# Optimization experiments

Hardware: AMD Instinct MI355X
Metric: run time of the kernel (lower is better)

## Reference

```python
import jax, jax.numpy as jnp
import numpy as np

B, S, D, H, L = 2, 4096, 768, 12, 12
DH = D // H
BS = 16                # block size
NB = S // BS           # 256 blocks
NR = 2                 # random blocks per middle query block
DFF = 3072
VOCAB = 50358


def layer_norm(x, s, b):
    m = x.mean(-1, keepdims=True)
    v = ((x - m) ** 2).mean(-1, keepdims=True)
    return (x - m) * jax.lax.rsqrt(v + 1e-12) * s + b


def setup_inputs() -> dict:
    key = jax.random.key(0)
    ks = jax.random.split(key, 20)
    rn = lambda k, shp: jax.random.normal(k, shp, jnp.float32) * 0.02
    # random key-block indices per middle query block, avoiding window+global blocks
    rng = np.random.default_rng(0)
    rb = np.zeros((NB - 2, NR), np.int32)
    for i in range(1, NB - 1):
        forbidden = {0, i - 1, i, i + 1, NB - 1}
        choices = np.array([b for b in range(NB) if b not in forbidden])
        rb[i - 1] = rng.choice(choices, NR, replace=False)
    return {
        "input_ids": jax.random.randint(ks[0], (B, S), 0, VOCAB, jnp.int32),
        "rand_blocks": jnp.asarray(rb),
        "emb_word": rn(ks[1], (VOCAB, D)),
        "emb_pos": rn(ks[2], (S, D)),
        "ln0_s": jnp.ones((D,)), "ln0_b": jnp.zeros((D,)),
        "Wq": rn(ks[3], (L, D, D)), "bq": jnp.zeros((L, D)),
        "Wk": rn(ks[4], (L, D, D)), "bk": jnp.zeros((L, D)),
        "Wv": rn(ks[5], (L, D, D)), "bv": jnp.zeros((L, D)),
        "Wo": rn(ks[6], (L, D, D)), "bo": jnp.zeros((L, D)),
        "ln1_s": jnp.ones((L, D)), "ln1_b": jnp.zeros((L, D)),
        "W1": rn(ks[7], (L, D, DFF)), "b1": jnp.zeros((L, DFF)),
        "W2": rn(ks[8], (L, DFF, D)), "b2": jnp.zeros((L, D)),
        "ln2_s": jnp.ones((L, D)), "ln2_b": jnp.zeros((L, D)),
        "Wp": rn(ks[9], (D, D)), "bp": jnp.zeros((D,)),
        "start_w": jax.random.normal(ks[10], (D,), jnp.float32),
        "end_w": jax.random.normal(ks[11], (D,), jnp.float32),
        "Wd1": rn(ks[12], (D, 20)), "bd1": jnp.zeros((20,)),
        "Wd2": rn(ks[13], (20, 2)), "bd2": jnp.zeros((2,)),
    }


def block_sparse_attn(h, wq, bq_, wk, bk_, wv, bv_, wo, bo_, rand_blocks):
    scale = 1.0 / np.sqrt(DH)
    heads = lambda w, b: (h @ w + b).reshape(B, S, H, DH).transpose(0, 2, 1, 3)
    q = heads(wq, bq_) * scale
    k = heads(wk, bk_)
    v = heads(wv, bv_)
    qb = q.reshape(B, H, NB, BS, DH)
    kb = k.reshape(B, H, NB, BS, DH)
    vb = v.reshape(B, H, NB, BS, DH)
    # global query blocks (first & last) attend to every key
    qg = qb[:, :, jnp.array([0, NB - 1])]                       # [B,H,2,BS,DH]
    ag = jax.nn.softmax(jnp.einsum('bhgqd,bhkd->bhgqk', qg, k), -1)
    og = jnp.einsum('bhgqk,bhkd->bhgqd', ag, v)
    # middle query blocks: global(2) + window(3) + random(2) key blocks
    mid = jnp.arange(1, NB - 1, dtype=jnp.int32)
    idx = jnp.concatenate([
        jnp.zeros((NB - 2, 1), jnp.int32),
        jnp.full((NB - 2, 1), NB - 1, jnp.int32),
        jnp.stack([mid - 1, mid, mid + 1], -1),
        rand_blocks.astype(jnp.int32),
    ], axis=1)                                                  # [NB-2, 7]
    kg = kb[:, :, idx].reshape(B, H, NB - 2, 7 * BS, DH)        # gathered keys
    vg = vb[:, :, idx].reshape(B, H, NB - 2, 7 * BS, DH)
    qm = qb[:, :, 1:NB - 1]                                     # [B,H,NB-2,BS,DH]
    am = jax.nn.softmax(jnp.einsum('bhnqd,bhnkd->bhnqk', qm, kg), -1)
    om = jnp.einsum('bhnqk,bhnkd->bhnqd', am, vg)
    ob = jnp.concatenate([og[:, :, :1], om, og[:, :, 1:]], axis=2)  # [B,H,NB,BS,DH]
    o = ob.reshape(B, H, S, DH).transpose(0, 2, 1, 3).reshape(B, S, D)
    return o @ wo + bo_


def encoder(input_ids, rand_blocks, emb_word, emb_pos, ln0_s, ln0_b,
            Wq, bq, Wk, bk, Wv, bv, Wo, bo, ln1_s, ln1_b,
            W1, b1, W2, b2, ln2_s, ln2_b):
    h = layer_norm(emb_word[input_ids] + emb_pos[None], ln0_s, ln0_b)

    def layer(hc, p):
        wq, bq_, wk, bk_, wv, bv_, wo, bo_, l1s, l1b, w1, b1_, w2, b2_, l2s, l2b = p
        a = block_sparse_attn(hc, wq, bq_, wk, bk_, wv, bv_, wo, bo_, rand_blocks)
        hc = layer_norm(hc + a, l1s, l1b)
        f = jax.nn.gelu(hc @ w1 + b1_, approximate=False) @ w2 + b2_
        hc = layer_norm(hc + f, l2s, l2b)
        return hc, None

    h, _ = jax.lax.scan(layer, h, (Wq, bq, Wk, bk, Wv, bv, Wo, bo,
                                   ln1_s, ln1_b, W1, b1, W2, b2, ln2_s, ln2_b))
    return h


def reference(input_ids, rand_blocks, emb_word, emb_pos, ln0_s, ln0_b,
              Wq, bq, Wk, bk, Wv, bv, Wo, bo, ln1_s, ln1_b,
              W1, b1, W2, b2, ln2_s, ln2_b, Wp, bp,
              start_w, end_w, Wd1, bd1, Wd2, bd2):
    h = encoder(input_ids, rand_blocks, emb_word, emb_pos, ln0_s, ln0_b,
                Wq, bq, Wk, bk, Wv, bv, Wo, bo, ln1_s, ln1_b,
                W1, b1, W2, b2, ln2_s, ln2_b)
    start_logits = h @ start_w        # [B,S]
    end_logits = h @ end_w            # [B,S]
    pooled = jnp.tanh(h[:, 0] @ Wp + bp)   # BERT-style pooler on [CLS]
    d1 = jax.nn.relu(pooled @ Wd1 + bd1)
    disc_logits = d1 @ Wd2 + bd2      # [B,2]
    return start_logits, end_logits, disc_logits
```

## Files before the change

### kernel.cpp

```cpp
#include <hip/hip_runtime.h>

#define DEV __device__ __forceinline__

typedef unsigned short u16;
typedef short bf16x8 __attribute__((ext_vector_type(8)));
typedef float f32x4 __attribute__((ext_vector_type(4)));

constexpr int Bc = 2, Sc = 4096, Dc = 768, Hc = 12, Lc = 12;
constexpr int BSc = 16, NBc = 256, NRc = 2, DFFc = 3072;
constexpr int Mr = Bc * Sc;

DEV u16 f2b(float f) {
  unsigned u = __builtin_bit_cast(unsigned, f);
  u += 0x7fffu + ((u >> 16) & 1u);
  return (u16)(u >> 16);
}
DEV float b2f(u16 u) { return __builtin_bit_cast(float, (unsigned)u << 16); }

DEV void gload_lds16(const void* g, void* l) {
  __builtin_amdgcn_global_load_lds((const __attribute__((address_space(1))) void*)g,
                                   (__attribute__((address_space(3))) void*)l, 16, 0, 0);
}

template<int EPI>
__global__ __launch_bounds__(512, 1)
void gemmP(const u16* __restrict__ A, const u16* __restrict__ Bt,
           const float* __restrict__ bias, u16* __restrict__ Cb,
           float* __restrict__ Cf,
           u16* __restrict__ Qh, u16* __restrict__ Kh, u16* __restrict__ Vh,
           u16* __restrict__ VhT, int M, int N, int K)
{
  __shared__ u16 As[2][128 * 64];
  __shared__ u16 Bs[2][256 * 64];
  const int tid = threadIdx.x;
  const int wid = tid >> 6, lane = tid & 63;
  const int fr = lane & 15, fq = lane >> 4;
  const int wr = wid >> 2, wc = wid & 3;

  int nwg = gridDim.x * gridDim.y;
  int orig = blockIdx.y * gridDim.x + blockIdx.x;
  int swz = (nwg & 7) ? orig : (orig & 7) * (nwg >> 3) + (orig >> 3);
  int bx = swz % gridDim.x, by = swz / gridDim.x;
  const int m0 = by * 128, n0 = bx * 256;

  const u16* asrc[2];
  const u16* bsrc[4];
#pragma unroll
  for (int p = 0; p < 2; ++p) {
    int ci = p * 512 + tid;
    int r = ci >> 3, c = (ci & 7) ^ (r & 7);
    asrc[p] = A + (size_t)(m0 + r) * K + c * 8;
  }
#pragma unroll
  for (int p = 0; p < 4; ++p) {
    int ci = p * 512 + tid;
    int r = ci >> 3, c = (ci & 7) ^ (r & 7);
    bsrc[p] = Bt + (size_t)(n0 + r) * K + c * 8;
  }
  auto stageA = [&](int buf, int k0) {
#pragma unroll
    for (int p = 0; p < 2; ++p)
      gload_lds16(asrc[p] + k0, &As[buf][(p * 512 + tid) * 8]);
  };
  auto stageB = [&](int buf, int k0) {
#pragma unroll
    for (int p = 0; p < 4; ++p)
      gload_lds16(bsrc[p] + k0, &Bs[buf][(p * 512 + tid) * 8]);
  };

  f32x4 acc[4][4] = {};
  const int arow = wr * 64 + fr;
  const int brow = wc * 64 + fr;

  stageA(0, 0);  stageB(0, 0);
  stageA(1, 64); stageB(1, 64);
  asm volatile("s_waitcnt vmcnt(6)" ::: "memory");
  __builtin_amdgcn_sched_barrier(0);
  __builtin_amdgcn_s_barrier();

  const int nt = K >> 6;
  for (int kt = 0; kt < nt; ++kt) {
    const u16* ab = As[kt & 1];
    const u16* bb = Bs[kt & 1];
    bf16x8 aA[2][2], aB[2][2], bA[2][2], bB[2][2];

#pragma unroll
    for (int f = 0; f < 2; ++f)
#pragma unroll
      for (int kh = 0; kh < 2; ++kh) {
        int rowa = arow + f * 16;
        aA[f][kh] = *(const bf16x8*)(ab + rowa * 64 + (((kh * 4 + fq) ^ (rowa & 7)) << 3));
        int rowb = brow + f * 16;
        bA[f][kh] = *(const bf16x8*)(bb + rowb * 64 + (((kh * 4 + fq) ^ (rowb & 7)) << 3));
      }
    __builtin_amdgcn_s_setprio(1);
#pragma unroll
    for (int m = 0; m < 2; ++m)
#pragma unroll
      for (int n = 0; n < 2; ++n)
#pragma unroll
        for (int kh = 0; kh < 2; ++kh)
          acc[m][n] = __builtin_amdgcn_mfma_f32_16x16x32_bf16(aA[m][kh], bA[n][kh], acc[m][n], 0, 0, 0);
    __builtin_amdgcn_s_setprio(0);

#pragma unroll
    for (int f = 0; f < 2; ++f)
#pragma unroll
      for (int kh = 0; kh < 2; ++kh) {
        int rowb = brow + 32 + f * 16;
        bB[f][kh] = *(const bf16x8*)(bb + rowb * 64 + (((kh * 4 + fq) ^ (rowb & 7)) << 3));
      }
    __builtin_amdgcn_s_setprio(1);
#pragma unroll
    for (int m = 0; m < 2; ++m)
#pragma unroll
      for (int n = 0; n < 2; ++n)
#pragma unroll
        for (int kh = 0; kh < 2; ++kh)
          acc[m][n + 2] = __builtin_amdgcn_mfma_f32_16x16x32_bf16(aA[m][kh], bB[n][kh], acc[m][n + 2], 0, 0, 0);
    __builtin_amdgcn_s_setprio(0);
    asm volatile("s_waitcnt lgkmcnt(0)" ::: "memory");
    __builtin_amdgcn_sched_barrier(0);
    __builtin_amdgcn_s_barrier();

    if (kt + 2 < nt) stageB(kt & 1, (kt + 2) * 64);
#pragma unroll
    for (int f = 0; f < 2; ++f)
#pragma unroll
      for (int kh = 0; kh < 2; ++kh) {
        int rowa = arow + 32 + f * 16;
        aB[f][kh] = *(const bf16x8*)(ab + rowa * 64 + (((kh * 4 + fq) ^ (rowa & 7)) << 3));
      }
    __builtin_amdgcn_s_setprio(1);
#pragma unroll
    for (int m = 0; m < 2; ++m)
#pragma unroll
      for (int n = 0; n < 2; ++n)
#pragma unroll
        for (int kh = 0; kh < 2; ++kh)
          acc[m + 2][n] = __builtin_amdgcn_mfma_f32_16x16x32_bf16(aB[m][kh], bA[n][kh], acc[m + 2][n], 0, 0, 0);
    __builtin_amdgcn_s_setprio(0);
    asm volatile("s_waitcnt lgkmcnt(0)" ::: "memory");
    __builtin_amdgcn_sched_barrier(0);
    __builtin_amdgcn_s_barrier();

    if (kt + 2 < nt) stageA(kt & 1, (kt + 2) * 64);
    __builtin_amdgcn_s_setprio(1);
#pragma unroll
    for (int m = 0; m < 2; ++m)
#pragma unroll
      for (int n = 0; n < 2; ++n)
#pragma unroll
        for (int kh = 0; kh < 2; ++kh)
          acc[m + 2][n + 2] = __builtin_amdgcn_mfma_f32_16x16x32_bf16(aB[m][kh], bB[n][kh], acc[m + 2][n + 2], 0, 0, 0);
    __builtin_amdgcn_s_setprio(0);
    if (kt + 1 < nt) {
      if (kt + 2 < nt) asm volatile("s_waitcnt vmcnt(6)" ::: "memory");
      else             asm volatile("s_waitcnt vmcnt(0)" ::: "memory");
      __builtin_amdgcn_sched_barrier(0);
      __builtin_amdgcn_s_barrier();
    }
  }

#pragma unroll
  for (int m = 0; m < 4; ++m) {
#pragma unroll
    for (int n = 0; n < 4; ++n) {
      int col = n0 + wc * 64 + n * 16 + fr;
      float bv = bias[col];
      if constexpr (EPI == 2) {
        int sec = col / 768;
        int c = col - sec * 768;
        int hh = c >> 6, dd = c & 63;
#pragma unroll
        for (int r = 0; r < 4; ++r) {
          int row = m0 + wr * 64 + m * 16 + fq * 4 + r;
          int bb2 = row >> 12, ss = row & 4095;
          size_t bhh = (size_t)(bb2 * Hc + hh);
          u16 val = f2b(acc[m][n][r] + bv);
          if (sec == 0) Qh[(bhh * Sc + ss) * 64 + dd] = val;
          else if (sec == 1) Kh[(bhh * Sc + ss) * 64 + dd] = val;
          else { Vh[(bhh * Sc + ss) * 64 + dd] = val; VhT[(bhh * 64 + dd) * Sc + ss] = val; }
        }
      } else if constexpr (EPI == 1) {
#pragma unroll
        for (int r = 0; r < 4; ++r) {
          int row = m0 + wr * 64 + m * 16 + fq * 4 + r;
          float v = acc[m][n][r] + bv;
          v = 0.5f * v * (1.f + erff(v * 0.70710678118654752f));
          Cb[(size_t)row * N + col] = f2b(v);
        }
      } else {
#pragma unroll
        for (int r = 0; r < 4; ++r) {
          int row = m0 + wr * 64 + m * 16 + fq * 4 + r;
          Cf[(size_t)row * N + col] = acc[m][n][r] + bv;
        }
      }
    }
  }
}

__global__ __launch_bounds__(256, 2)
void gemmQ(const u16* __restrict__ A, const u16* __restrict__ Bt,
           const float* __restrict__ bias, float* __restrict__ Cf,
           int M, int N, int K)
{
  __shared__ u16 As[2][128 * 64];
  __shared__ u16 Bs[2][128 * 64];
  const int tid = threadIdx.x;
  const int wid = tid >> 6, lane = tid & 63;
  const int fr = lane & 15, fq = lane >> 4;
  const int wr = wid >> 1, wc = wid & 1;

  int nwg = gridDim.x * gridDim.y;
  int orig = blockIdx.y * gridDim.x + blockIdx.x;
  int swz = (nwg & 7) ? orig : (orig & 7) * (nwg >> 3) + (orig >> 3);
  int bx = swz % gridDim.x, by = swz / gridDim.x;
  const int m0 = by * 128, n0 = bx * 128;

  const u16* asrc[4];
  const u16* bsrc[4];
#pragma unroll
  for (int p = 0; p < 4; ++p) {
    int ci = p * 256 + tid;
    int r = ci >> 3, c = (ci & 7) ^ (r & 7);
    asrc[p] = A + (size_t)(m0 + r) * K + c * 8;
    bsrc[p] = Bt + (size_t)(n0 + r) * K + c * 8;
  }
  auto stageA = [&](int buf, int k0) {
#pragma unroll
    for (int p = 0; p < 4; ++p)
      gload_lds16(asrc[p] + k0, &As[buf][(p * 256 + tid) * 8]);
  };
  auto stageB = [&](int buf, int k0) {
#pragma unroll
    for (int p = 0; p < 4; ++p)
      gload_lds16(bsrc[p] + k0, &Bs[buf][(p * 256 + tid) * 8]);
  };

  f32x4 acc[4][4] = {};
  const int arow = wr * 64 + fr;
  const int brow = wc * 64 + fr;

  stageA(0, 0);  stageB(0, 0);
  stageA(1, 64); stageB(1, 64);
  asm volatile("s_waitcnt vmcnt(8)" ::: "memory");
  __builtin_amdgcn_sched_barrier(0);
  __builtin_amdgcn_s_barrier();

  const int nt = K >> 6;
  for (int kt = 0; kt < nt; ++kt) {
    const u16* ab = As[kt & 1];
    const u16* bb = Bs[kt & 1];
    bf16x8 aA[2][2], aB[2][2], bA[2][2], bB[2][2];

#pragma unroll
    for (int f = 0; f < 2; ++f)
#pragma unroll
      for (int kh = 0; kh < 2; ++kh) {
        int rowa = arow + f * 16;
        aA[f][kh] = *(const bf16x8*)(ab + rowa * 64 + (((kh * 4 + fq) ^ (rowa & 7)) << 3));
        int rowb = brow + f * 16;
        bA[f][kh] = *(const bf16x8*)(bb + rowb * 64 + (((kh * 4 + fq) ^ (rowb & 7)) << 3));
      }
    __builtin_amdgcn_s_setprio(1);
#pragma unroll
    for (int m = 0; m < 2; ++m)
#pragma unroll
      for (int n = 0; n < 2; ++n)
#pragma unroll
        for (int kh = 0; kh < 2; ++kh)
          acc[m][n] = __builtin_amdgcn_mfma_f32_16x16x32_bf16(aA[m][kh], bA[n][kh], acc[m][n], 0, 0, 0);
    __builtin_amdgcn_s_setprio(0);

#pragma unroll
    for (int f = 0; f < 2; ++f)
#pragma unroll
      for (int kh = 0; kh < 2; ++kh) {
        int rowb = brow + 32 + f * 16;
        bB[f][kh] = *(const bf16x8*)(bb + rowb * 64 + (((kh * 4 + fq) ^ (rowb & 7)) << 3));
      }
    __builtin_amdgcn_s_setprio(1);
#pragma unroll
    for (int m = 0; m < 2; ++m)
#pragma unroll
      for (int n = 0; n < 2; ++n)
#pragma unroll
        for (int kh = 0; kh < 2; ++kh)
          acc[m][n + 2] = __builtin_amdgcn_mfma_f32_16x16x32_bf16(aA[m][kh], bB[n][kh], acc[m][n + 2], 0, 0, 0);
    __builtin_amdgcn_s_setprio(0);
    asm volatile("s_waitcnt lgkmcnt(0)" ::: "memory");
    __builtin_amdgcn_sched_barrier(0);
    __builtin_amdgcn_s_barrier();

    if (kt + 2 < nt) stageB(kt & 1, (kt + 2) * 64);
#pragma unroll
    for (int f = 0; f < 2; ++f)
#pragma unroll
      for (int kh = 0; kh < 2; ++kh) {
        int rowa = arow + 32 + f * 16;
        aB[f][kh] = *(const bf16x8*)(ab + rowa * 64 + (((kh * 4 + fq) ^ (rowa & 7)) << 3));
      }
    __builtin_amdgcn_s_setprio(1);
#pragma unroll
    for (int m = 0; m < 2; ++m)
#pragma unroll
      for (int n = 0; n < 2; ++n)
#pragma unroll
        for (int kh = 0; kh < 2; ++kh)
          acc[m + 2][n] = __builtin_amdgcn_mfma_f32_16x16x32_bf16(aB[m][kh], bA[n][kh], acc[m + 2][n], 0, 0, 0);
    __builtin_amdgcn_s_setprio(0);
    asm volatile("s_waitcnt lgkmcnt(0)" ::: "memory");
    __builtin_amdgcn_sched_barrier(0);
    __builtin_amdgcn_s_barrier();

    if (kt + 2 < nt) stageA(kt & 1, (kt + 2) * 64);
    __builtin_amdgcn_s_setprio(1);
#pragma unroll
    for (int m = 0; m < 2; ++m)
#pragma unroll
      for (int n = 0; n < 2; ++n)
#pragma unroll
        for (int kh = 0; kh < 2; ++kh)
          acc[m + 2][n + 2] = __builtin_amdgcn_mfma_f32_16x16x32_bf16(aB[m][kh], bB[n][kh], acc[m + 2][n + 2], 0, 0, 0);
    __builtin_amdgcn_s_setprio(0);
    if (kt + 1 < nt) {
      if (kt + 2 < nt) asm volatile("s_waitcnt vmcnt(8)" ::: "memory");
      else             asm volatile("s_waitcnt vmcnt(0)" ::: "memory");
      __builtin_amdgcn_sched_barrier(0);
      __builtin_amdgcn_s_barrier();
    }
  }

#pragma unroll
  for (int m = 0; m < 4; ++m) {
#pragma unroll
    for (int n = 0; n < 4; ++n) {
      int col = n0 + wc * 64 + n * 16 + fr;
      float bv = bias[col];
#pragma unroll
      for (int r = 0; r < 4; ++r) {
        int row = m0 + wr * 64 + m * 16 + fq * 4 + r;
        Cf[(size_t)row * N + col] = acc[m][n][r] + bv;
      }
    }
  }
}

__global__ void wtrans_all(const float* __restrict__ Wq, const float* __restrict__ Wk,
                           const float* __restrict__ Wv, const float* __restrict__ Wo,
                           const float* __restrict__ W1, const float* __restrict__ W2,
                           u16* __restrict__ wqkvT, u16* __restrict__ woT,
                           u16* __restrict__ w1T, u16* __restrict__ w2T)
{
  int bx = blockIdx.x;
  size_t l = blockIdx.y;
  size_t wsq = l * 768 * 768, wff = l * 768 * 3072;
  const float* in; u16* out; int K, N, ntx, t; float scale = 1.f;
  if (bx < 576)       { in = Wq + wsq; out = wqkvT + l * 2304 * 768;           K = 768;  N = 768;  ntx = 24; t = bx;        scale = 0.125f; }
  else if (bx < 1152) { in = Wk + wsq; out = wqkvT + l * 2304 * 768 + 589824;  K = 768;  N = 768;  ntx = 24; t = bx - 576;  }
  else if (bx < 1728) { in = Wv + wsq; out = wqkvT + l * 2304 * 768 + 1179648; K = 768;  N = 768;  ntx = 24; t = bx - 1152; }
  else if (bx < 2304) { in = Wo + wsq; out = woT + l * 768 * 768;              K = 768;  N = 768;  ntx = 24; t = bx - 1728; }
  else if (bx < 4608) { in = W1 + wff; out = w1T + l * 3072 * 768;             K = 768;  N = 3072; ntx = 96; t = bx - 2304; }
  else                { in = W2 + wff; out = w2T + l * 768 * 3072;             K = 3072; N = 768;  ntx = 24; t = bx - 4608; }
  int n0 = (t % ntx) * 32, k0 = (t / ntx) * 32;
  __shared__ float tl[32][33];
  int tx = threadIdx.x, ty = threadIdx.y;
#pragma unroll
  for (int yy = 0; yy < 32; yy += 8)
    tl[ty + yy][tx] = in[(size_t)(k0 + ty + yy) * N + n0 + tx];
  __syncthreads();
#pragma unroll
  for (int yy = 0; yy < 32; yy += 8)
    out[(size_t)(n0 + ty + yy) * K + k0 + tx] = f2b(tl[tx][ty + yy] * scale);
}

__global__ void pack_bias(const float* __restrict__ bq, const float* __restrict__ bk,
                          const float* __restrict__ bv, float* __restrict__ bqkv)
{
  int i = blockIdx.x * 256 + threadIdx.x;
  if (i >= Lc * 2304) return;
  int l = i / 2304, j = i % 2304;
  float v = (j < 768) ? bq[(size_t)l * 768 + j] * 0.125f
          : (j < 1536) ? bk[(size_t)l * 768 + j - 768]
                       : bv[(size_t)l * 768 + j - 1536];
  bqkv[i] = v;
}

DEV void breduce2(float& a, float& b) {
  __shared__ float ra[4], rbv[4];
  for (int off = 32; off > 0; off >>= 1) {
    a += __shfl_down(a, off);
    b += __shfl_down(b, off);
  }
  int lane = threadIdx.x & 63, wid = threadIdx.x >> 6;
  if (lane == 0) { ra[wid] = a; rbv[wid] = b; }
  __syncthreads();
  a = ra[0] + ra[1] + ra[2] + ra[3];
  b = rbv[0] + rbv[1] + rbv[2] + rbv[3];
}

__global__ __launch_bounds__(256)
void embed_ln(const int* __restrict__ ids, const float* __restrict__ ew,
              const float* __restrict__ ep, const float* __restrict__ gs,
              const float* __restrict__ gb, float* __restrict__ hout, u16* __restrict__ hb)
{
  int row = blockIdx.x;
  int spos = row & (Sc - 1);
  int id = ids[row];
  int tid = threadIdx.x;
  float x[3], sum = 0.f, ss = 0.f;
#pragma unroll
  for (int j = 0; j < 3; ++j) {
    int i = tid + j * 256;
    x[j] = ew[(size_t)id * Dc + i] + ep[(size_t)spos * Dc + i];
    sum += x[j]; ss += x[j] * x[j];
  }
  breduce2(sum, ss);
  float mean = sum * (1.f / Dc);
  float var = ss * (1.f / Dc) - mean * mean;
  float inv = rsqrtf(var + 1e-12f);
#pragma unroll
  for (int j = 0; j < 3; ++j) {
    int i = tid + j * 256;
    float y = (x[j] - mean) * inv * gs[i] + gb[i];
    hout[(size_t)row * Dc + i] = y;
    hb[(size_t)row * Dc + i] = f2b(y);
  }
}

__global__ __launch_bounds__(256)
void ln_res(const float* X, const float* R, const float* gs, const float* gb,
            float* Yf, u16* Yb)
{
  int row = blockIdx.x;
  int tid = threadIdx.x;
  float x[3], sum = 0.f, ss = 0.f;
#pragma unroll
  for (int j = 0; j < 3; ++j) {
    int i = tid + j * 256;
    x[j] = X[(size_t)row * Dc + i] + R[(size_t)row * Dc + i];
    sum += x[j]; ss += x[j] * x[j];
  }
  breduce2(sum, ss);
  float mean = sum * (1.f / Dc);
  float var = ss * (1.f / Dc) - mean * mean;
  float inv = rsqrtf(var + 1e-12f);
#pragma unroll
  for (int j = 0; j < 3; ++j) {
    int i = tid + j * 256;
    float y = (x[j] - mean) * inv * gs[i] + gb[i];
    Yf[(size_t)row * Dc + i] = y;
    Yb[(size_t)row * Dc + i] = f2b(y);
  }
}

__global__ __launch_bounds__(256)
void gattn_flash(const u16* __restrict__ Qh, const u16* __restrict__ Kh,
                 const u16* __restrict__ VhT, float* __restrict__ part)
{
  __shared__ u16 pb[4][16 * 136];
  __shared__ float ob[4][16][64];
  __shared__ float mlb[4][2][16];
  const int kc = blockIdx.x, g = blockIdx.y, bh = blockIdx.z;
  const int wid = threadIdx.x >> 6, lane = threadIdx.x & 63;
  const int fr = lane & 15, fq = lane >> 4;
  const int qrow = g ? (NBc - 1) * BSc : 0;

  const u16* Qb = Qh + ((size_t)bh * Sc + qrow) * 64;
  const u16* Kb = Kh + (size_t)bh * Sc * 64;
  const u16* Vt = VhT + (size_t)bh * 64 * Sc;

  bf16x8 qa0 = *(const bf16x8*)(Qb + fr * 64 + fq * 8);
  bf16x8 qa1 = *(const bf16x8*)(Qb + fr * 64 + 32 + fq * 8);

  float m[4], l[4];
  f32x4 o[4] = {};
#pragma unroll
  for (int r = 0; r < 4; ++r) { m[r] = -3.4e38f; l[r] = 0.f; }

  u16* pbw = pb[wid];
  const int s0w = kc * 256 + wid * 64;

  for (int it = 0; it < 2; ++it) {
    const int sb = s0w + it * 32;
    f32x4 s[2];
#pragma unroll
    for (int t = 0; t < 2; ++t) {
      const u16* kr = Kb + (size_t)(sb + t * 16 + fr) * 64 + fq * 8;
      bf16x8 kb0 = *(const bf16x8*)(kr);
      bf16x8 kb1 = *(const bf16x8*)(kr + 32);
      f32x4 a = {};
      a = __builtin_amdgcn_mfma_f32_16x16x32_bf16(qa0, kb0, a, 0, 0, 0);
      a = __builtin_amdgcn_mfma_f32_16x16x32_bf16(qa1, kb1, a, 0, 0, 0);
      s[t] = a;
    }
#pragma unroll
    for (int r = 0; r < 4; ++r) {
      float pm = fmaxf(s[0][r], s[1][r]);
#pragma unroll
      for (int off = 1; off < 16; off <<= 1) pm = fmaxf(pm, __shfl_xor(pm, off));
      float nm = fmaxf(m[r], pm);
      float sc = __expf(m[r] - nm);
      m[r] = nm;
      float e0 = __expf(s[0][r] - nm), e1 = __expf(s[1][r] - nm);
      float ps = e0 + e1;
#pragma unroll
      for (int off = 1; off < 16; off <<= 1) ps += __shfl_xor(ps, off);
      l[r] = l[r] * sc + ps;
#pragma unroll
      for (int nn = 0; nn < 4; ++nn) o[nn][r] *= sc;
      pbw[(fq * 4 + r) * 136 + fr] = f2b(e0);
      pbw[(fq * 4 + r) * 136 + 16 + fr] = f2b(e1);
    }
    asm volatile("s_waitcnt lgkmcnt(0)" ::: "memory");
    __builtin_amdgcn_sched_barrier(0);
    bf16x8 pa = *(const bf16x8*)(pbw + fr * 136 + fq * 8);
#pragma unroll
    for (int nn = 0; nn < 4; ++nn) {
      bf16x8 vb = *(const bf16x8*)(Vt + (size_t)(nn * 16 + fr) * Sc + sb + fq * 8);
      o[nn] = __builtin_amdgcn_mfma_f32_16x16x32_bf16(pa, vb, o[nn], 0, 0, 0);
    }
  }

#pragma unroll
  for (int nn = 0; nn < 4; ++nn)
#pragma unroll
    for (int r = 0; r < 4; ++r)
      ob[wid][fq * 4 + r][nn * 16 + fr] = o[nn][r];
  if (fr == 0) {
#pragma unroll
    for (int r = 0; r < 4; ++r) {
      mlb[wid][0][fq * 4 + r] = m[r];
      mlb[wid][1][fq * 4 + r] = l[r];
    }
  }
  __syncthreads();

  float* pp = part + (size_t)(((bh * 2 + g) * 16) + kc) * 1056;
  int tid = threadIdx.x;
#pragma unroll
  for (int k = 0; k < 4; ++k) {
    int oidx = tid + k * 256;
    int q = oidx >> 6, d = oidx & 63;
    float M = fmaxf(fmaxf(mlb[0][0][q], mlb[1][0][q]), fmaxf(mlb[2][0][q], mlb[3][0][q]));
    float O = 0.f, L = 0.f;
#pragma unroll
    for (int w = 0; w < 4; ++w) {
      float f = __expf(mlb[w][0][q] - M);
      O += f * ob[w][q][d];
      L += f * mlb[w][1][q];
    }
    pp[q * 64 + d] = O;
    if (d == 0) { pp[1024 + q] = M; pp[1040 + q] = L; }
  }
}

__global__ __launch_bounds__(256)
void attn_tail(const u16* __restrict__ Qh, const u16* __restrict__ Kh,
               const u16* __restrict__ VhT, const int* __restrict__ rb,
               const float* __restrict__ part, u16* __restrict__ attnb)
{
  if (blockIdx.x < 48) {
    int idx = blockIdx.x;
    int bh = idx >> 1, g = idx & 1;
    int b = bh / Hc, h = bh % Hc;
    int tid = threadIdx.x;
    const float* pbase = part + (size_t)idx * 16 * 1056;
#pragma unroll
    for (int k = 0; k < 4; ++k) {
      int oidx = tid + k * 256;
      int q = oidx >> 6, d = oidx & 63;
      float M = -3.4e38f;
#pragma unroll
      for (int c = 0; c < 16; ++c) M = fmaxf(M, pbase[c * 1056 + 1024 + q]);
      float O = 0.f, L = 0.f;
#pragma unroll
      for (int c = 0; c < 16; ++c) {
        float f = __expf(pbase[c * 1056 + 1024 + q] - M);
        O += f * pbase[c * 1056 + q * 64 + d];
        L += f * pbase[c * 1056 + 1040 + q];
      }
      int srow = (g ? (NBc - 1) * BSc : 0) + q;
      attnb[((size_t)(b * Sc + srow)) * Dc + h * 64 + d] = f2b(O / L);
    }
    return;
  }

  __shared__ u16 pb[4][16 * 136];
  const int wid = threadIdx.x >> 6, lane = threadIdx.x & 63;
  const int w = (blockIdx.x - 48) * 4 + wid;
  const int n = w % 254, bh = w / 254;
  const int b = bh / Hc, h = bh % Hc;
  const int fr = lane & 15, fq = lane >> 4;

  int idx[7];
  idx[0] = 0; idx[1] = NBc - 1; idx[2] = n; idx[3] = n + 1; idx[4] = n + 2;
  idx[5] = rb[n * NRc]; idx[6] = rb[n * NRc + 1];

  const u16* Qb = Qh + ((size_t)bh * Sc + (n + 1) * BSc) * 64;
  const u16* Kb = Kh + (size_t)bh * Sc * 64;
  const u16* Vt = VhT + (size_t)bh * 64 * Sc;

  bf16x8 qa0 = *(const bf16x8*)(Qb + fr * 64 + fq * 8);
  bf16x8 qa1 = *(const bf16x8*)(Qb + fr * 64 + 32 + fq * 8);

  f32x4 s[7];
#pragma unroll
  for (int t = 0; t < 7; ++t) {
    const u16* kr = Kb + ((size_t)idx[t] * BSc + fr) * 64 + fq * 8;
    bf16x8 kb0 = *(const bf16x8*)(kr);
    bf16x8 kb1 = *(const bf16x8*)(kr + 32);
    f32x4 a = {};
    a = __builtin_amdgcn_mfma_f32_16x16x32_bf16(qa0, kb0, a, 0, 0, 0);
    a = __builtin_amdgcn_mfma_f32_16x16x32_bf16(qa1, kb1, a, 0, 0, 0);
    s[t] = a;
  }

  float mx[4], sm[4];
#pragma unroll
  for (int r = 0; r < 4; ++r) {
    mx[r] = s[0][r];
#pragma unroll
    for (int t = 1; t < 7; ++t) mx[r] = fmaxf(mx[r], s[t][r]);
  }
#pragma unroll
  for (int off = 1; off < 16; off <<= 1)
#pragma unroll
    for (int r = 0; r < 4; ++r) mx[r] = fmaxf(mx[r], __shfl_xor(mx[r], off));
#pragma unroll
  for (int r = 0; r < 4; ++r) sm[r] = 0.f;
#pragma unroll
  for (int t = 0; t < 7; ++t)
#pragma unroll
    for (int r = 0; r < 4; ++r) { float e = expf(s[t][r] - mx[r]); s[t][r] = e; sm[r] += e; }
#pragma unroll
  for (int off = 1; off < 16; off <<= 1)
#pragma unroll
    for (int r = 0; r < 4; ++r) sm[r] += __shfl_xor(sm[r], off);
  float inv[4];
#pragma unroll
  for (int r = 0; r < 4; ++r) inv[r] = 1.f / sm[r];

  u16* pbw = pb[wid];
#pragma unroll
  for (int t = 0; t < 7; ++t)
#pragma unroll
    for (int r = 0; r < 4; ++r)
      pbw[(fq * 4 + r) * 136 + t * 16 + fr] = f2b(s[t][r] * inv[r]);
  for (int i = lane; i < 16 * 24; i += 64) {
    int rr = i / 24, cc = 112 + i % 24;
    pbw[rr * 136 + cc] = 0;
  }
  __syncthreads();

  f32x4 o[4] = {};
#pragma unroll
  for (int ks = 0; ks < 4; ++ks) {
    bf16x8 pa = *(const bf16x8*)(pbw + fr * 136 + ks * 32 + fq * 8);
    int t = ks * 2 + (fq >> 1);
    int tt = (t < 7) ? t : 0;
    size_t voff = (size_t)idx[tt] * BSc + (fq & 1) * 8;
#pragma unroll
    for (int nn = 0; nn < 4; ++nn) {
      bf16x8 vb = *(const bf16x8*)(Vt + (size_t)(nn * 16 + fr) * Sc + voff);
      o[nn] = __builtin_amdgcn_mfma_f32_16x16x32_bf16(pa, vb, o[nn], 0, 0, 0);
    }
  }

  size_t rbase = (size_t)b * Sc + (n + 1) * BSc;
#pragma unroll
  for (int nn = 0; nn < 4; ++nn)
#pragma unroll
    for (int r = 0; r < 4; ++r)
      attnb[(rbase + fq * 4 + r) * Dc + h * 64 + nn * 16 + fr] = f2b(o[nn][r]);
}

__global__ __launch_bounds__(256)
void logits_k(const float* __restrict__ h, const float* __restrict__ sw,
              const float* __restrict__ ew, float* __restrict__ out)
{
  int row = blockIdx.x;
  int tid = threadIdx.x;
  float s1 = 0.f, s2 = 0.f;
#pragma unroll
  for (int j = 0; j < 3; ++j) {
    int i = tid + j * 256;
    float x = h[(size_t)row * Dc + i];
    s1 += x * sw[i]; s2 += x * ew[i];
  }
  breduce2(s1, s2);
  if (tid == 0) { out[row] = s1; out[Mr + row] = s2; }
}

__global__ __launch_bounds__(256)
void pooled_k(const float* __restrict__ h, const float* __restrict__ Wp,
              const float* __restrict__ bp, float* __restrict__ pooled)
{
  int b = blockIdx.y, j0 = blockIdx.x * 64;
  int jl = threadIdx.x & 63, kp = threadIdx.x >> 6;
  __shared__ float hr[768];
  __shared__ float part[4][64];
  for (int i = threadIdx.x; i < 768; i += 256) hr[i] = h[(size_t)b * Sc * Dc + i];
  __syncthreads();
  float a0 = 0.f, a1 = 0.f, a2 = 0.f, a3 = 0.f;
  const float* wp = Wp + (size_t)(kp * 192) * 768 + j0 + jl;
  const float* hk = hr + kp * 192;
#pragma unroll 4
  for (int k = 0; k < 192; k += 4) {
    a0 += hk[k]     * wp[(size_t)k * 768];
    a1 += hk[k + 1] * wp[(size_t)(k + 1) * 768];
    a2 += hk[k + 2] * wp[(size_t)(k + 2) * 768];
    a3 += hk[k + 3] * wp[(size_t)(k + 3) * 768];
  }
  part[kp][jl] = a0 + a1 + a2 + a3;
  __syncthreads();
  if (threadIdx.x < 64) {
    float s = part[0][jl] + part[1][jl] + part[2][jl] + part[3][jl] + bp[j0 + jl];
    pooled[b * 768 + j0 + jl] = tanhf(s);
  }
}

__global__ __launch_bounds__(256)
void head2(const float* __restrict__ pooled, const float* __restrict__ Wd1,
           const float* __restrict__ bd1, const float* __restrict__ Wd2,
           const float* __restrict__ bd2, float* __restrict__ out)
{
  __shared__ float pl[1536];
  __shared__ float part[40][6];
  __shared__ float d1[40];
  int tid = threadIdx.x;
  for (int i = tid; i < 1536; i += 256) pl[i] = pooled[i];
  __syncthreads();
  if (tid < 240) {
    int p = tid / 6, s = tid % 6;
    int b = p / 20, u = p % 20;
    float a = 0.f;
    for (int k = s * 128; k < s * 128 + 128; ++k) a += pl[b * 768 + k] * Wd1[(size_t)k * 20 + u];
    part[p][s] = a;
  }
  __syncthreads();
  if (tid < 40) {
    float a = bd1[tid % 20];
#pragma unroll
    for (int s = 0; s < 6; ++s) a += part[tid][s];
    d1[tid] = fmaxf(a, 0.f);
  }
  __syncthreads();
  if (tid < 4) {
    int b = tid >> 1, o = tid & 1;
    float a = bd2[o];
#pragma unroll
    for (int k = 0; k < 20; ++k) a += d1[b * 20 + k] * Wd2[k * 2 + o];
    out[2 * Mr + b * 2 + o] = a;
  }
}

extern "C" void kernel_launch(void* const* d_in, const int* in_sizes, int n_in,
                              void* d_out, int out_size, void* d_ws, size_t ws_size,
                              hipStream_t stream)
{
  (void)in_sizes; (void)n_in; (void)out_size; (void)ws_size;
  const int*   ids   = (const int*)d_in[0];
  const int*   rbp   = (const int*)d_in[1];
  const float* emb_w = (const float*)d_in[2];
  const float* emb_p = (const float*)d_in[3];
  const float* ln0s  = (const float*)d_in[4];
  const float* ln0b  = (const float*)d_in[5];
  const float* Wq    = (const float*)d_in[6];
  const float* bq    = (const float*)d_in[7];
  const float* Wk    = (const float*)d_in[8];
  const float* bk    = (const float*)d_in[9];
  const float* Wv    = (const float*)d_in[10];
  const float* bv    = (const float*)d_in[11];
  const float* Wo    = (const float*)d_in[12];
  const float* bo    = (const float*)d_in[13];
  const float* ln1s  = (const float*)d_in[14];
  const float* ln1b  = (const float*)d_in[15];
  const float* W1    = (const float*)d_in[16];
  const float* b1    = (const float*)d_in[17];
  const float* W2    = (const float*)d_in[18];
  const float* b2    = (const float*)d_in[19];
  const float* ln2s  = (const float*)d_in[20];
  const float* ln2b  = (const float*)d_in[21];
  const float* Wp    = (const float*)d_in[22];
  const float* bp    = (const float*)d_in[23];
  const float* sw    = (const float*)d_in[24];
  const float* ewv   = (const float*)d_in[25];
  const float* Wd1   = (const float*)d_in[26];
  const float* bd1   = (const float*)d_in[27];
  const float* Wd2   = (const float*)d_in[28];
  const float* bd2   = (const float*)d_in[29];
  float* out = (float*)d_out;

  unsigned char* pc = (unsigned char*)d_ws;
  auto carve = [&](size_t bytes) {
    void* r = (void*)pc;
    pc += (bytes + 255) & ~(size_t)255;
    return r;
  };
  u16*   wqkvT = (u16*)carve((size_t)Lc * 2304 * 768 * 2);
  u16*   woT   = (u16*)carve((size_t)Lc * 768 * 768 * 2);
  u16*   w1T   = (u16*)carve((size_t)Lc * 3072 * 768 * 2);
  u16*   w2T   = (u16*)carve((size_t)Lc * 768 * 3072 * 2);
  float* bqkv  = (float*)carve((size_t)Lc * 2304 * 4);
  float* h     = (float*)carve((size_t)Mr * Dc * 4);
  u16*   hb    = (u16*)carve((size_t)Mr * Dc * 2);
  u16*   Qh    = (u16*)carve((size_t)Mr * Dc * 2);
  u16*   Kh    = (u16*)carve((size_t)Mr * Dc * 2);
  u16*   Vh    = (u16*)carve((size_t)Mr * Dc * 2);
  u16*   VhT   = (u16*)carve((size_t)Mr * Dc * 2);
  u16*   attnb = (u16*)carve((size_t)Mr * Dc * 2);
  float* c0    = (float*)carve((size_t)Mr * Dc * 4);
  float* pool2 = (float*)carve((size_t)Bc * Dc * 4);
  float* m1ws  = (float*)carve((size_t)Mr * DFFc * 2);
  u16*   m1    = (u16*)m1ws;
  float* part  = (float*)((unsigned char*)m1ws + (size_t)13 * 1024 * 1024);

  pack_bias<<<(Lc * 2304 + 255) / 256, 256, 0, stream>>>(bq, bk, bv, bqkv);
  wtrans_all<<<dim3(6912, Lc), dim3(32, 8), 0, stream>>>(Wq, Wk, Wv, Wo, W1, W2,
                                                         wqkvT, woT, w1T, w2T);
  embed_ln<<<Mr, 256, 0, stream>>>(ids, emb_w, emb_p, ln0s, ln0b, h, hb);

  for (int l = 0; l < Lc; ++l) {
    gemmP<2><<<dim3(9, 64), 512, 0, stream>>>(hb, wqkvT + (size_t)l * 2304 * 768,
                                              bqkv + (size_t)l * 2304,
                                              nullptr, nullptr, Qh, Kh, Vh, VhT, Mr, 2304, 768);
    gattn_flash<<<dim3(16, 2, Bc * Hc), 256, 0, stream>>>(Qh, Kh, VhT, part);
    attn_tail<<<48 + 1524, 256, 0, stream>>>(Qh, Kh, VhT, rbp, part, attnb);
    gemmQ<<<dim3(6, 64), 256, 0, stream>>>(attnb, woT + (size_t)l * 768 * 768,
                                           bo + (size_t)l * 768, c0, Mr, 768, 768);
    ln_res<<<Mr, 256, 0, stream>>>(h, c0, ln1s + (size_t)l * 768, ln1b + (size_t)l * 768, h, hb);
    gemmP<1><<<dim3(12, 64), 512, 0, stream>>>(hb, w1T + (size_t)l * 3072 * 768,
                                               b1 + (size_t)l * 3072,
                                               m1, nullptr, nullptr, nullptr, nullptr, nullptr,
                                               Mr, 3072, 768);
    gemmQ<<<dim3(6, 64), 256, 0, stream>>>(m1, w2T + (size_t)l * 768 * 3072,
                                           b2 + (size_t)l * 768, c0, Mr, 768, 3072);
    ln_res<<<Mr, 256, 0, stream>>>(h, c0, ln2s + (size_t)l * 768, ln2b + (size_t)l * 768, h, hb);
  }

  logits_k<<<Mr, 256, 0, stream>>>(h, sw, ewv, out);
  pooled_k<<<dim3(12, Bc), 256, 0, stream>>>(h, Wp, bp, pool2);
  head2<<<1, 256, 0, stream>>>(pool2, Wd1, bd1, Wd2, bd2, out);
}
```

Measured before the change: 3.703 ms.

## Cut memory traffic: drop Vh, bf16 GEMM outputs, vectorize LN and weight transpose

The QKV epilogue no longer writes the unused row-major V copy, and the output-projection and FFN2 GEMMs now store bf16 instead of fp32 into the residual buffer. ln_res is rewritten to process one row per wavefront with float4/ushort4 vector loads and a shuffle-only reduction. The weight transpose kernel moves to 64x64 tiles with vectorized loads and packed stores. Rounding the residual branch to bf16 before the add loses some precision in exchange for less memory traffic.

```diff
diff --git a/kernel.cpp b/kernel.cpp
--- a/kernel.cpp
+++ b/kernel.cpp
@@ -26,8 +26,7 @@
 __global__ __launch_bounds__(512, 1)
 void gemmP(const u16* __restrict__ A, const u16* __restrict__ Bt,
            const float* __restrict__ bias, u16* __restrict__ Cb,
-           float* __restrict__ Cf,
-           u16* __restrict__ Qh, u16* __restrict__ Kh, u16* __restrict__ Vh,
+           u16* __restrict__ Qh, u16* __restrict__ Kh,
            u16* __restrict__ VhT, int M, int N, int K)
 {
   __shared__ u16 As[2][128 * 64];
@@ -180,9 +179,9 @@
           u16 val = f2b(acc[m][n][r] + bv);
           if (sec == 0) Qh[(bhh * Sc + ss) * 64 + dd] = val;
           else if (sec == 1) Kh[(bhh * Sc + ss) * 64 + dd] = val;
-          else { Vh[(bhh * Sc + ss) * 64 + dd] = val; VhT[(bhh * 64 + dd) * Sc + ss] = val; }
+          else VhT[(bhh * 64 + dd) * Sc + ss] = val;
         }
-      } else if constexpr (EPI == 1) {
+      } else {
 #pragma unroll
         for (int r = 0; r < 4; ++r) {
           int row = m0 + wr * 64 + m * 16 + fq * 4 + r;
@@ -190,12 +189,6 @@
           v = 0.5f * v * (1.f + erff(v * 0.70710678118654752f));
           Cb[(size_t)row * N + col] = f2b(v);
         }
-      } else {
-#pragma unroll
-        for (int r = 0; r < 4; ++r) {
-          int row = m0 + wr * 64 + m * 16 + fq * 4 + r;
-          Cf[(size_t)row * N + col] = acc[m][n][r] + bv;
-        }
       }
     }
   }
@@ -203,7 +196,7 @@
 
 __global__ __launch_bounds__(256, 2)
 void gemmQ(const u16* __restrict__ A, const u16* __restrict__ Bt,
-           const float* __restrict__ bias, float* __restrict__ Cf,
+           const float* __restrict__ bias, u16* __restrict__ Cb,
            int M, int N, int K)
 {
   __shared__ u16 As[2][128 * 64];
@@ -342,38 +335,47 @@
 #pragma unroll
       for (int r = 0; r < 4; ++r) {
         int row = m0 + wr * 64 + m * 16 + fq * 4 + r;
-        Cf[(size_t)row * N + col] = acc[m][n][r] + bv;
+        Cb[(size_t)row * N + col] = f2b(acc[m][n][r] + bv);
       }
     }
   }
 }
 
-__global__ void wtrans_all(const float* __restrict__ Wq, const float* __restrict__ Wk,
-                           const float* __restrict__ Wv, const float* __restrict__ Wo,
-                           const float* __restrict__ W1, const float* __restrict__ W2,
-                           u16* __restrict__ wqkvT, u16* __restrict__ woT,
-                           u16* __restrict__ w1T, u16* __restrict__ w2T)
+__global__ __launch_bounds__(256)
+void wtrans_all(const float* __restrict__ Wq, const float* __restrict__ Wk,
+                const float* __restrict__ Wv, const float* __restrict__ Wo,
+                const float* __restrict__ W1, const float* __restrict__ W2,
+                u16* __restrict__ wqkvT, u16* __restrict__ woT,
+                u16* __restrict__ w1T, u16* __restrict__ w2T)
 {
   int bx = blockIdx.x;
   size_t l = blockIdx.y;
   size_t wsq = l * 768 * 768, wff = l * 768 * 3072;
   const float* in; u16* out; int K, N, ntx, t; float scale = 1.f;
-  if (bx < 576)       { in = Wq + wsq; out = wqkvT + l * 2304 * 768;           K = 768;  N = 768;  ntx = 24; t = bx;        scale = 0.125f; }
-  else if (bx < 1152) { in = Wk + wsq; out = wqkvT + l * 2304 * 768 + 589824;  K = 768;  N = 768;  ntx = 24; t = bx - 576;  }
-  else if (bx < 1728) { in = Wv + wsq; out = wqkvT + l * 2304 * 768 + 1179648; K = 768;  N = 768;  ntx = 24; t = bx - 1152; }
-  else if (bx < 2304) { in = Wo + wsq; out = woT + l * 768 * 768;              K = 768;  N = 768;  ntx = 24; t = bx - 1728; }
-  else if (bx < 4608) { in = W1 + wff; out = w1T + l * 3072 * 768;             K = 768;  N = 3072; ntx = 96; t = bx - 2304; }
-  else                { in = W2 + wff; out = w2T + l * 768 * 3072;             K = 3072; N = 768;  ntx = 24; t = bx - 4608; }
-  int n0 = (t % ntx) * 32, k0 = (t / ntx) * 32;
-  __shared__ float tl[32][33];
-  int tx = threadIdx.x, ty = threadIdx.y;
-#pragma unroll
-  for (int yy = 0; yy < 32; yy += 8)
-    tl[ty + yy][tx] = in[(size_t)(k0 + ty + yy) * N + n0 + tx];
+  if (bx < 144)       { in = Wq + wsq; out = wqkvT + l * 2304 * 768;           K = 768;  N = 768;  ntx = 12; t = bx;        scale = 0.125f; }
+  else if (bx < 288)  { in = Wk + wsq; out = wqkvT + l * 2304 * 768 + 589824;  K = 768;  N = 768;  ntx = 12; t = bx - 144;  }
+  else if (bx < 432)  { in = Wv + wsq; out = wqkvT + l * 2304 * 768 + 1179648; K = 768;  N = 768;  ntx = 12; t = bx - 288;  }
+  else if (bx < 576)  { in = Wo + wsq; out = woT + l * 768 * 768;              K = 768;  N = 768;  ntx = 12; t = bx - 432;  }
+  else if (bx < 1152) { in = W1 + wff; out = w1T + l * 3072 * 768;             K = 768;  N = 3072; ntx = 48; t = bx - 576;  }
+  else                { in = W2 + wff; out = w2T + l * 768 * 3072;             K = 3072; N = 768;  ntx = 12; t = bx - 1152; }
+  int n0 = (t % ntx) * 64, k0 = (t / ntx) * 64;
+  __shared__ float tl[64][65];
+  int tid = threadIdx.x;
+  int kr = tid >> 4, nc = (tid & 15) * 4;
+#pragma unroll
+  for (int kk = 0; kk < 4; ++kk) {
+    float4 v = *(const float4*)(in + (size_t)(k0 + kk * 16 + kr) * N + n0 + nc);
+    float* d = &tl[kk * 16 + kr][nc];
+    d[0] = v.x; d[1] = v.y; d[2] = v.z; d[3] = v.w;
+  }
   __syncthreads();
-#pragma unroll
-  for (int yy = 0; yy < 32; yy += 8)
-    out[(size_t)(n0 + ty + yy) * K + k0 + tx] = f2b(tl[tx][ty + yy] * scale);
+  int k2 = (tid & 31) * 2, nr = tid >> 5;
+#pragma unroll
+  for (int nn = 0; nn < 8; ++nn) {
+    int n = nn * 8 + nr;
+    unsigned pk = (unsigned)f2b(tl[k2][n] * scale) | ((unsigned)f2b(tl[k2 + 1][n] * scale) << 16);
+    *(unsigned*)(out + (size_t)(n0 + n) * K + k0 + k2) = pk;
+  }
 }
 
 __global__ void pack_bias(const float* __restrict__ bq, const float* __restrict__ bk,
@@ -431,28 +433,50 @@
 }
 
 __global__ __launch_bounds__(256)
-void ln_res(const float* X, const float* R, const float* gs, const float* gb,
-            float* Yf, u16* Yb)
-{
-  int row = blockIdx.x;
-  int tid = threadIdx.x;
-  float x[3], sum = 0.f, ss = 0.f;
-#pragma unroll
-  for (int j = 0; j < 3; ++j) {
-    int i = tid + j * 256;
-    x[j] = X[(size_t)row * Dc + i] + R[(size_t)row * Dc + i];
-    sum += x[j]; ss += x[j] * x[j];
-  }
-  breduce2(sum, ss);
+void ln_res(const float* __restrict__ X, const u16* __restrict__ Rb,
+            const float* __restrict__ gs, const float* __restrict__ gb,
+            float* __restrict__ Yf, u16* __restrict__ Yb)
+{
+  const int wid = threadIdx.x >> 6, lane = threadIdx.x & 63;
+  const int row = blockIdx.x * 4 + wid;
+  const float* xr = X + (size_t)row * Dc;
+  const u16*   rr = Rb + (size_t)row * Dc;
+  float x[12];
+  float sum = 0.f, ss = 0.f;
+#pragma unroll
+  for (int p = 0; p < 3; ++p) {
+    int c = p * 256 + lane * 4;
+    float4 xv = *(const float4*)(xr + c);
+    ushort4 rv = *(const ushort4*)(rr + c);
+    float v0 = xv.x + b2f(rv.x);
+    float v1 = xv.y + b2f(rv.y);
+    float v2 = xv.z + b2f(rv.z);
+    float v3 = xv.w + b2f(rv.w);
+    x[p * 4 + 0] = v0; x[p * 4 + 1] = v1; x[p * 4 + 2] = v2; x[p * 4 + 3] = v3;
+    sum += (v0 + v1) + (v2 + v3);
+    ss  += (v0 * v0 + v1 * v1) + (v2 * v2 + v3 * v3);
+  }
+#pragma unroll
+  for (int off = 1; off < 64; off <<= 1) {
+    sum += __shfl_xor(sum, off);
+    ss  += __shfl_xor(ss, off);
+  }
   float mean = sum * (1.f / Dc);
   float var = ss * (1.f / Dc) - mean * mean;
   float inv = rsqrtf(var + 1e-12f);
 #pragma unroll
-  for (int j = 0; j < 3; ++j) {
-    int i = tid + j * 256;
-    float y = (x[j] - mean) * inv * gs[i] + gb[i];
-    Yf[(size_t)row * Dc + i] = y;
-    Yb[(size_t)row * Dc + i] = f2b(y);
+  for (int p = 0; p < 3; ++p) {
+    int c = p * 256 + lane * 4;
+    float4 gv = *(const float4*)(gs + c);
+    float4 bv = *(const float4*)(gb + c);
+    float y0 = (x[p * 4 + 0] - mean) * inv * gv.x + bv.x;
+    float y1 = (x[p * 4 + 1] - mean) * inv * gv.y + bv.y;
+    float y2 = (x[p * 4 + 2] - mean) * inv * gv.z + bv.z;
+    float y3 = (x[p * 4 + 3] - mean) * inv * gv.w + bv.w;
+    float4 yo; yo.x = y0; yo.y = y1; yo.z = y2; yo.w = y3;
+    *(float4*)(Yf + (size_t)row * Dc + c) = yo;
+    ushort4 pk; pk.x = f2b(y0); pk.y = f2b(y1); pk.z = f2b(y2); pk.w = f2b(y3);
+    *(ushort4*)(Yb + (size_t)row * Dc + c) = pk;
   }
 }
 
@@ -809,36 +833,35 @@
   u16*   hb    = (u16*)carve((size_t)Mr * Dc * 2);
   u16*   Qh    = (u16*)carve((size_t)Mr * Dc * 2);
   u16*   Kh    = (u16*)carve((size_t)Mr * Dc * 2);
-  u16*   Vh    = (u16*)carve((size_t)Mr * Dc * 2);
   u16*   VhT   = (u16*)carve((size_t)Mr * Dc * 2);
   u16*   attnb = (u16*)carve((size_t)Mr * Dc * 2);
-  float* c0    = (float*)carve((size_t)Mr * Dc * 4);
+  u16*   c0b   = (u16*)carve((size_t)Mr * Dc * 2);
   float* pool2 = (float*)carve((size_t)Bc * Dc * 4);
   float* m1ws  = (float*)carve((size_t)Mr * DFFc * 2);
   u16*   m1    = (u16*)m1ws;
   float* part  = (float*)((unsigned char*)m1ws + (size_t)13 * 1024 * 1024);
 
   pack_bias<<<(Lc * 2304 + 255) / 256, 256, 0, stream>>>(bq, bk, bv, bqkv);
-  wtrans_all<<<dim3(6912, Lc), dim3(32, 8), 0, stream>>>(Wq, Wk, Wv, Wo, W1, W2,
-                                                         wqkvT, woT, w1T, w2T);
+  wtrans_all<<<dim3(1728, Lc), 256, 0, stream>>>(Wq, Wk, Wv, Wo, W1, W2,
+                                                 wqkvT, woT, w1T, w2T);
   embed_ln<<<Mr, 256, 0, stream>>>(ids, emb_w, emb_p, ln0s, ln0b, h, hb);
 
   for (int l = 0; l < Lc; ++l) {
     gemmP<2><<<dim3(9, 64), 512, 0, stream>>>(hb, wqkvT + (size_t)l * 2304 * 768,
                                               bqkv + (size_t)l * 2304,
-                                              nullptr, nullptr, Qh, Kh, Vh, VhT, Mr, 2304, 768);
+                                              nullptr, Qh, Kh, VhT, Mr, 2304, 768);
     gattn_flash<<<dim3(16, 2, Bc * Hc), 256, 0, stream>>>(Qh, Kh, VhT, part);
     attn_tail<<<48 + 1524, 256, 0, stream>>>(Qh, Kh, VhT, rbp, part, attnb);
     gemmQ<<<dim3(6, 64), 256, 0, stream>>>(attnb, woT + (size_t)l * 768 * 768,
-                                           bo + (size_t)l * 768, c0, Mr, 768, 768);
-    ln_res<<<Mr, 256, 0, stream>>>(h, c0, ln1s + (size_t)l * 768, ln1b + (size_t)l * 768, h, hb);
+                                           bo + (size_t)l * 768, c0b, Mr, 768, 768);
+    ln_res<<<Mr / 4, 256, 0, stream>>>(h, c0b, ln1s + (size_t)l * 768, ln1b + (size_t)l * 768, h, hb);
     gemmP<1><<<dim3(12, 64), 512, 0, stream>>>(hb, w1T + (size_t)l * 3072 * 768,
                                                b1 + (size_t)l * 3072,
-                                               m1, nullptr, nullptr, nullptr, nullptr, nullptr,
+                                               m1, nullptr, nullptr, nullptr,
                                                Mr, 3072, 768);
     gemmQ<<<dim3(6, 64), 256, 0, stream>>>(m1, w2T + (size_t)l * 768 * 3072,
-                                           b2 + (size_t)l * 768, c0, Mr, 768, 3072);
-    ln_res<<<Mr, 256, 0, stream>>>(h, c0, ln2s + (size_t)l * 768, ln2b + (size_t)l * 768, h, hb);
+                                           b2 + (size_t)l * 768, c0b, Mr, 768, 3072);
+    ln_res<<<Mr / 4, 256, 0, stream>>>(h, c0b, ln2s + (size_t)l * 768, ln2b + (size_t)l * 768, h, hb);
   }
 
   logits_k<<<Mr, 256, 0, stream>>>(h, sw, ewv, out);
```

After: 3.582 ms. 1.03x faster.
